# Optimization experiments

Hardware: AMD Instinct MI355X
Metric: run time of the kernel (lower is better)

The kernel has to match this reference:

```python
import jax, jax.numpy as jnp
import numpy as np
import math

NUM_CONVS = 4
GN_GROUPS = 32
GN_EPS = 1e-5
FPN_STRIDES = (8, 16, 32, 64, 128)
PRIOR_PROB = 0.01


def conv3x3(x, w, b):
    # x: [N,C,H,W], w: [O,I,3,3]
    y = jax.lax.conv_general_dilated(
        x, w, window_strides=(1, 1), padding='SAME',
        dimension_numbers=('NCHW', 'OIHW', 'NCHW'))
    return y + b[None, :, None, None]


def group_norm(x, gamma, beta):
    n, c, h, w = x.shape
    xg = x.reshape(n, GN_GROUPS, c // GN_GROUPS, h, w)
    mean = xg.mean(axis=(2, 3, 4), keepdims=True)
    var = xg.var(axis=(2, 3, 4), keepdims=True)
    xn = ((xg - mean) * jax.lax.rsqrt(var + GN_EPS)).reshape(n, c, h, w)
    return xn * gamma[None, :, None, None] + beta[None, :, None, None]


def subnet(x, ws, bs, gws, gbs):
    # NUM_CONVS x (conv3x3 -> GN -> ReLU)
    for i in range(NUM_CONVS):
        x = jax.nn.relu(group_norm(conv3x3(x, ws[i], bs[i]), gws[i], gbs[i]))
    return x


def permute_to_N_HWA_K(x, k):
    n = x.shape[0]
    return x.transpose(0, 2, 3, 1).reshape(n, -1, k)


def setup_inputs() -> dict:
    key = jax.random.key(0)
    ks = jax.random.split(key, 16)
    C, K = 256, 80
    feats = {
        'p3': jax.random.normal(ks[0], (1, C, 80, 80), jnp.float32),
        'p4': jax.random.normal(ks[1], (1, C, 40, 40), jnp.float32),
        'p5': jax.random.normal(ks[2], (1, C, 20, 20), jnp.float32),
        'p6': jax.random.normal(ks[3], (1, C, 10, 10), jnp.float32),
        'p7': jax.random.normal(ks[4], (1, C, 5, 5), jnp.float32),
    }
    std = 0.01
    bias_value = -math.log((1 - PRIOR_PROB) / PRIOR_PROB)
    params = {
        'cls_w': std * jax.random.normal(ks[5], (NUM_CONVS, C, C, 3, 3), jnp.float32),
        'cls_b': jnp.zeros((NUM_CONVS, C), jnp.float32),
        'cls_gn_w': jnp.ones((NUM_CONVS, C), jnp.float32),
        'cls_gn_b': jnp.zeros((NUM_CONVS, C), jnp.float32),
        'box_w': std * jax.random.normal(ks[6], (NUM_CONVS, C, C, 3, 3), jnp.float32),
        'box_b': jnp.zeros((NUM_CONVS, C), jnp.float32),
        'box_gn_w': jnp.ones((NUM_CONVS, C), jnp.float32),
        'box_gn_b': jnp.zeros((NUM_CONVS, C), jnp.float32),
        'score_w': std * jax.random.normal(ks[7], (K, C, 3, 3), jnp.float32),
        'score_b': jnp.full((K,), bias_value, jnp.float32),
        'pred_w': std * jax.random.normal(ks[8], (4, C, 3, 3), jnp.float32),
        'pred_b': jnp.zeros((4,), jnp.float32),
        'iou_w': std * jax.random.normal(ks[9], (1, C, 3, 3), jnp.float32),
        'iou_b': jnp.zeros((1,), jnp.float32),
        'scales': jnp.ones((5,), jnp.float32),
    }
    return {**feats, **params}


def reference(p3, p4, p5, p6, p7,
              cls_w, cls_b, cls_gn_w, cls_gn_b,
              box_w, box_b, box_gn_w, box_gn_b,
              score_w, score_b, pred_w, pred_b, iou_w, iou_b, scales):
    features = [p3, p4, p5, p6, p7]
    logits, bbox_reg, ious = [], [], []
    for l, feat in enumerate(features):
        c = subnet(feat, cls_w, cls_b, cls_gn_w, cls_gn_b)
        b = subnet(feat, box_w, box_b, box_gn_w, box_gn_b)
        logit = conv3x3(c, score_w, score_b)          # [N,80,H,W]
        iou = conv3x3(b, iou_w, iou_b)                # [N,1,H,W]
        bp = conv3x3(b, pred_w, pred_b) * scales[l]   # Scale module
        # norm_reg_targets=True branch
        reg = jax.nn.relu(bp) * FPN_STRIDES[l]        # [N,4,H,W]
        logits.append(permute_to_N_HWA_K(logit, 80))
        bbox_reg.append(permute_to_N_HWA_K(reg, 4))
        ious.append(permute_to_N_HWA_K(iou, 1))
    box_cls = jnp.concatenate(logits, axis=1)    # [N, sumHW, 80]
    box_delta = jnp.concatenate(bbox_reg, axis=1)  # [N, sumHW, 4]
    box_iou = jnp.concatenate(ious, axis=1)      # [N, sumHW, 1]
    # pack into one array for a single output: [N, sumHW, 85]
    return jnp.concatenate([box_cls, box_delta, box_iou], axis=-1)
```

## Files before the change

### kernel.cpp

```cpp
#include <hip/hip_runtime.h>

typedef unsigned short u16;
typedef __attribute__((ext_vector_type(8))) short bf16x8;
typedef __attribute__((ext_vector_type(4))) float f32x4;

#define NLEV 5
#define CCH 256
#define KTOT 2304
#define P_TOT 8525
#define PP_TOT 9165

__constant__ int   c_HW[NLEV]     = {6400, 1600, 400, 100, 25};
__constant__ int   c_W[NLEV]      = {80, 40, 20, 10, 5};
__constant__ int   c_off[NLEV]    = {0, 6400, 8000, 8400, 8500};
__constant__ int   c_poff[NLEV]   = {0, 6724, 8488, 8972, 9116};
__constant__ int   c_pts[NLEV+1]  = {0, 100, 125, 132, 134, 135};
__constant__ float c_stridef[NLEV]= {8.f, 16.f, 32.f, 64.f, 128.f};

__device__ __forceinline__ u16 f2bf(float f){
  union { float f; unsigned u; } v; v.f = f;
  unsigned r = v.u + 0x7fffu + ((v.u >> 16) & 1u);
  return (u16)(r >> 16);
}

__device__ __forceinline__ void g2l16(const u16* g, u16* l, int lane){
#if defined(__has_builtin)
#if __has_builtin(__builtin_amdgcn_global_load_lds)
  __builtin_amdgcn_global_load_lds(
      (const __attribute__((address_space(1))) unsigned int*)g,
      (__attribute__((address_space(3))) unsigned int*)l, 16, 0, 0);
  return;
#endif
#endif
  *(uint4*)(l + lane*8) = *(const uint4*)g;
}

#define WAIT_VM0   0x0F70
#define WAIT_LGKM0 0xC07F

template<int MODE>
__global__ __launch_bounds__(256, 2) void gemm_conv(
    const u16* __restrict__ Xc, const u16* __restrict__ Xb,
    const u16* __restrict__ Wc, const u16* __restrict__ Wb,
    const float* __restrict__ bc, const float* __restrict__ bb,
    float* __restrict__ Yc, float* __restrict__ Yb,
    float* __restrict__ stats,
    const float* __restrict__ predb, const float* __restrict__ ioub,
    const float* __restrict__ scales, float* __restrict__ out)
{
  __shared__ u16 sbuf[4*8192];
  __shared__ float sstat[32][2];

  const int ptile = blockIdx.x, br = blockIdx.z;
  const int tid = threadIdx.x, wv = tid >> 6, ln = tid & 63;

  if (MODE == 1) {
    if (br == 0 ? (wv >= 2) : (wv >= 1)) return;
  }

  int lv = 0;
  #pragma unroll
  for (int i = 1; i < NLEV; i++) if (ptile >= c_pts[i]) lv = i;
  const int ptl = ptile - c_pts[lv];
  const int HW = c_HW[lv], Wl = c_W[lv], wrow = Wl + 2;
  const int quad = ln >> 4, l15 = ln & 15;
  const int lr = ln >> 3;
  const int gsw = (ln & 7) ^ lr;

  const u16* __restrict__ X  = br ? Xb : Xc;
  const u16* __restrict__ WA = br ? Wb : Wc;

  u16* myA = &sbuf[wv * 8192];
  u16* myB = myA + 4096;

  const u16* aptr[8]; const u16* bptr[8];
  #pragma unroll
  for (int j = 0; j < 8; j++)
    aptr[j] = WA + (size_t)(wv*64 + j*8 + lr) * KTOT + gsw*8;
  #pragma unroll
  for (int j = 0; j < 8; j++) {
    const int p = ptl*64 + j*8 + lr;
    int pb = 0;
    if (p < HW) { const int h = p / Wl, wi = p - h*Wl; pb = h*wrow + wi; }
    bptr[j] = X + (size_t)(c_poff[lv] + pb) * CCH + gsw*8;
  }

  auto stage = [&](int s) {
    const int tap = s >> 2;
    const int dh = tap / 3, dw = tap - dh*3;
    const int aof = s * 64;
    const int bof = (dh*wrow + dw)*CCH + ((s & 3) << 6);
    #pragma unroll
    for (int j = 0; j < 8; j++) g2l16(aptr[j] + aof, myA + j*512, ln);
    #pragma unroll
    for (int j = 0; j < 8; j++) g2l16(bptr[j] + bof, myB + j*512, ln);
  };

  f32x4 acc[4][4];
  #pragma unroll
  for (int i = 0; i < 4; i++)
    #pragma unroll
    for (int j = 0; j < 4; j++) acc[i][j] = (f32x4){0.f, 0.f, 0.f, 0.f};

  stage(0);
  #pragma unroll 1
  for (int s = 0; s < 36; s++) {
    __builtin_amdgcn_s_waitcnt(WAIT_VM0);
    bf16x8 af[2][4], bf[2][4];
    #pragma unroll
    for (int sub = 0; sub < 2; sub++) {
      const int ga = ((sub*4 + quad) ^ (l15 & 7)) * 8;
      #pragma unroll
      for (int t = 0; t < 4; t++) {
        af[sub][t] = *(const bf16x8*)&myA[(t*16 + l15)*64 + ga];
        bf[sub][t] = *(const bf16x8*)&myB[(t*16 + l15)*64 + ga];
      }
    }
    __builtin_amdgcn_s_waitcnt(WAIT_LGKM0);
    if (s < 35) stage(s + 1);
    #pragma unroll
    for (int sub = 0; sub < 2; sub++)
      #pragma unroll
      for (int mt = 0; mt < 4; mt++)
        #pragma unroll
        for (int nt = 0; nt < 4; nt++)
          acc[mt][nt] = __builtin_amdgcn_mfma_f32_16x16x32_bf16(
              af[sub][mt], bf[sub][nt], acc[mt][nt], 0, 0, 0);
  }

  const int nrem = HW - ptl*64;
  if (MODE == 0) {
    if (tid < 64) sstat[tid >> 1][tid & 1] = 0.f;
    __syncthreads();
    const float* __restrict__ bias = br ? bb : bc;
    float* __restrict__ Y = br ? Yb : Yc;
    #pragma unroll
    for (int mt = 0; mt < 4; mt++) {
      const int mrow = wv*64 + mt*16 + quad*4;
      const f32x4 bv = *(const f32x4*)&bias[mrow];
      float s = 0.f, sq = 0.f;
      #pragma unroll
      for (int nt = 0; nt < 4; nt++) {
        const int nl = nt*16 + l15;
        f32x4 v = acc[mt][nt] + bv;
        if (nl < nrem) {
          const size_t n = (size_t)(c_off[lv] + ptl*64 + nl);
          *(f32x4*)&Y[n*CCH + mrow] = v;
          #pragma unroll
          for (int r = 0; r < 4; r++) { s += v[r]; sq += v[r]*v[r]; }
        }
      }
      #pragma unroll
      for (int o = 1; o < 16; o <<= 1) { s += __shfl_xor(s, o); sq += __shfl_xor(sq, o); }
      if (l15 == 0) {
        const int g = mrow >> 3;
        atomicAdd(&sstat[g][0], s);
        atomicAdd(&sstat[g][1], sq);
      }
    }
    __syncthreads();
    if (tid < 64) {
      const int g = tid >> 1, c = tid & 1;
      atomicAdd(&stats[((br*NLEV + lv)*32 + g)*2 + c], sstat[g][c]);
    }
  } else {
    const float scl = scales[lv];
    const float stf = c_stridef[lv];
    #pragma unroll
    for (int mt = 0; mt < 4; mt++) {
      const int mr0 = wv*64 + mt*16 + quad*4;
      if (mr0 >= 85) continue;
      #pragma unroll
      for (int nt = 0; nt < 4; nt++) {
        const int nl = nt*16 + l15;
        if (nl >= nrem) continue;
        const size_t n = (size_t)(c_off[lv] + ptl*64 + nl);
        const f32x4 v = acc[mt][nt];
        #pragma unroll
        for (int r = 0; r < 4; r++) {
          const int m = mr0 + r;
          if (br == 0) {
            if (m < 80) out[n*85 + m] = v[r] + bc[m];
          } else {
            if (m < 4) {
              const float t = (v[r] + predb[m]) * scl;
              out[n*85 + 80 + m] = fmaxf(t, 0.f) * stf;
            } else if (m == 4) {
              out[n*85 + 84] = v[r] + ioub[0];
            }
          }
        }
      }
    }
  }
}

__global__ __launch_bounds__(256) void gn_relu(
    const float* __restrict__ Yc, const float* __restrict__ Yb,
    const float* __restrict__ stats,
    const float* __restrict__ gwc, const float* __restrict__ gbc,
    const float* __restrict__ gwb, const float* __restrict__ gbb,
    u16* __restrict__ Xc, u16* __restrict__ Xb)
{
  const int t = blockIdx.x * 256 + threadIdx.x;
  if (t >= 2 * P_TOT * 32) return;
  const int br = t / (P_TOT * 32);
  const int r  = t - br * (P_TOT * 32);
  const int pg = r >> 5;
  const int c0 = (r & 31) << 3;
  int lv = 0;
  #pragma unroll
  for (int i = 1; i < NLEV; i++) if (pg >= c_off[i]) lv = i;
  const int pl = pg - c_off[lv];
  const int Wl = c_W[lv];
  const int g = c0 >> 3;
  const float* st = &stats[(((size_t)br*NLEV + lv)*32 + g)*2];
  const float cnt = 8.f * (float)c_HW[lv];
  const float mean = st[0] / cnt;
  const float var  = st[1] / cnt - mean*mean;
  const float rstd = rsqrtf(var + 1e-5f);
  const float* Y  = br ? Yb : Yc;
  const float* gw = br ? gwb : gwc;
  const float* gb = br ? gbb : gbc;
  u16* X = br ? Xb : Xc;
  const float* y = &Y[(size_t)pg*CCH + c0];
  const int h = pl / Wl, wi = pl - h*Wl;
  const size_t pidx = (size_t)(c_poff[lv] + (h+1)*(Wl+2) + (wi+1));
  union { u16 u[8]; uint4 v; } pk;
  #pragma unroll
  for (int i = 0; i < 8; i++) {
    const float v = (y[i] - mean)*rstd*gw[c0+i] + gb[c0+i];
    pk.u[i] = f2bf(fmaxf(v, 0.f));
  }
  *(uint4*)&X[pidx*CCH + c0] = pk.v;
}

__global__ __launch_bounds__(256) void feat2bf(
    const float* __restrict__ p3, const float* __restrict__ p4,
    const float* __restrict__ p5, const float* __restrict__ p6,
    const float* __restrict__ p7, u16* __restrict__ X)
{
  const int t = blockIdx.x * 256 + threadIdx.x;
  if (t >= P_TOT * 32) return;
  const int pg = t >> 5, c0 = (t & 31) << 3;
  int lv = 0;
  #pragma unroll
  for (int i = 1; i < NLEV; i++) if (pg >= c_off[i]) lv = i;
  const int pl = pg - c_off[lv];
  const float* src = lv==0 ? p3 : lv==1 ? p4 : lv==2 ? p5 : lv==3 ? p6 : p7;
  const int HW = c_HW[lv], Wl = c_W[lv];
  const int h = pl / Wl, wi = pl - h*Wl;
  const size_t pidx = (size_t)(c_poff[lv] + (h+1)*(Wl+2) + (wi+1));
  union { u16 u[8]; uint4 v; } pk;
  #pragma unroll
  for (int i = 0; i < 8; i++)
    pk.u[i] = f2bf(src[(size_t)(c0+i)*HW + pl]);
  *(uint4*)&X[pidx*CCH + c0] = pk.v;
}

__global__ __launch_bounds__(256) void wconv(
    const float* __restrict__ cw, const float* __restrict__ bw,
    u16* __restrict__ Wc, u16* __restrict__ Wb)
{
  const size_t N = (size_t)4*256*KTOT;
  const size_t t = (size_t)blockIdx.x * 256 + threadIdx.x;
  if (t >= 2*N) return;
  const float* src = (t < N) ? cw : bw;
  u16* dst = (t < N) ? Wc : Wb;
  const size_t i = (t < N) ? t : t - N;
  const size_t lc = i / KTOT;
  const int kk = (int)(i - lc*KTOT);
  const int tap = kk >> 8, ci = kk & 255;
  dst[i] = f2bf(src[(lc*256 + ci)*9 + tap]);
}

__global__ __launch_bounds__(256) void hconv(
    const float* __restrict__ sw, const float* __restrict__ pw,
    const float* __restrict__ iw, u16* __restrict__ Whc, u16* __restrict__ Whb)
{
  const int N = 128 * KTOT;
  const int t = blockIdx.x * 256 + threadIdx.x;
  if (t >= 2*N) return;
  const int i = (t < N) ? t : t - N;
  const int co = i / KTOT, kk = i - co*KTOT;
  const int tap = kk >> 8, ci = kk & 255;
  float v = 0.f;
  if (t < N) {
    if (co < 80) v = sw[(co*256 + ci)*9 + tap];
    Whc[i] = f2bf(v);
  } else {
    if (co < 4)       v = pw[(co*256 + ci)*9 + tap];
    else if (co == 4) v = iw[ci*9 + tap];
    Whb[i] = f2bf(v);
  }
}

extern "C" void kernel_launch(void* const* d_in, const int* in_sizes, int n_in,
                              void* d_out, int out_size, void* d_ws, size_t ws_size,
                              hipStream_t stream)
{
  const float* p3      = (const float*)d_in[0];
  const float* p4      = (const float*)d_in[1];
  const float* p5      = (const float*)d_in[2];
  const float* p6      = (const float*)d_in[3];
  const float* p7      = (const float*)d_in[4];
  const float* cls_w   = (const float*)d_in[5];
  const float* cls_b   = (const float*)d_in[6];
  const float* cls_gw  = (const float*)d_in[7];
  const float* cls_gb  = (const float*)d_in[8];
  const float* box_w   = (const float*)d_in[9];
  const float* box_b   = (const float*)d_in[10];
  const float* box_gw  = (const float*)d_in[11];
  const float* box_gb  = (const float*)d_in[12];
  const float* score_w = (const float*)d_in[13];
  const float* score_b = (const float*)d_in[14];
  const float* pred_w  = (const float*)d_in[15];
  const float* pred_b  = (const float*)d_in[16];
  const float* iou_w   = (const float*)d_in[17];
  const float* iou_b   = (const float*)d_in[18];
  const float* scales  = (const float*)d_in[19];
  float* out = (float*)d_out;

  char* w = (char*)d_ws;
  size_t o = 0;
  auto alloc = [&](size_t b) { void* p = w + o; o += (b + 255) & ~(size_t)255; return p; };
  u16*   XF = (u16*)alloc((size_t)PP_TOT*CCH*2);
  u16*   XC = (u16*)alloc((size_t)PP_TOT*CCH*2);
  u16*   XB = (u16*)alloc((size_t)PP_TOT*CCH*2);
  float* ST = (float*)alloc((size_t)4*2*NLEV*32*2*4);
  u16*  WRC = (u16*)alloc((size_t)4*256*KTOT*2);
  u16*  WRB = (u16*)alloc((size_t)4*256*KTOT*2);
  u16*  WHC = (u16*)alloc((size_t)128*KTOT*2);
  u16*  WHB = (u16*)alloc((size_t)128*KTOT*2);
  float* YC = (float*)alloc((size_t)P_TOT*CCH*4);
  float* YB = (float*)alloc((size_t)P_TOT*CCH*4);

  hipMemsetAsync(XF, 0, (size_t)3*PP_TOT*CCH*2 + (size_t)4*2*NLEV*32*2*4, stream);

  wconv<<<dim3((unsigned)(((size_t)2*4*256*KTOT + 255)/256)), 256, 0, stream>>>(cls_w, box_w, WRC, WRB);
  hconv<<<dim3((2*128*KTOT + 255)/256), 256, 0, stream>>>(score_w, pred_w, iou_w, WHC, WHB);
  feat2bf<<<dim3((P_TOT*32 + 255)/256), 256, 0, stream>>>(p3, p4, p5, p6, p7, XF);

  const u16* xci = XF; const u16* xbi = XF;
  for (int l = 0; l < 4; l++) {
    float* STl = ST + (size_t)l*2*NLEV*32*2;
    gemm_conv<0><<<dim3(135, 1, 2), 256, 0, stream>>>(
        xci, xbi, WRC + (size_t)l*256*KTOT, WRB + (size_t)l*256*KTOT,
        cls_b + l*256, box_b + l*256, YC, YB, STl,
        nullptr, nullptr, nullptr, nullptr);
    gn_relu<<<dim3((2*P_TOT*32 + 255)/256), 256, 0, stream>>>(
        YC, YB, STl, cls_gw + l*256, cls_gb + l*256, box_gw + l*256, box_gb + l*256,
        XC, XB);
    xci = XC; xbi = XB;
  }
  gemm_conv<1><<<dim3(135, 1, 2), 256, 0, stream>>>(
      xci, xbi, WHC, WHB, score_b, nullptr, nullptr, nullptr, nullptr,
      pred_b, iou_b, scales, out);
}
```

Measured before the change: 396.6 us.

## Share 128x128 LDS tiles across waves with double buffering and blocked layouts

The conv GEMM moves from per-wave private 64x64 tiles to a block-shared 128(M)x128(N) tile. All four waves cooperatively load A and B into double-buffered LDS and synchronise with a barrier each stage, so each loaded tile is reused across waves. Weights are pre-swizzled into a stage-blocked layout, and activations are stored channel-blocked in groups of 64, so each stage's loads are contiguous. This cuts redundant global and LDS traffic per output, but adds a per-stage barrier and reduces the block count (69x2x2 for the body convs, 69x1x2 for the heads), which may hurt occupancy on the small levels.

```diff
diff --git a/kernel.cpp b/kernel.cpp
--- a/kernel.cpp
+++ b/kernel.cpp
@@ -9,12 +9,13 @@
 #define KTOT 2304
 #define P_TOT 8525
 #define PP_TOT 9165
+#define PLS (PP_TOT*64)
 
 __constant__ int   c_HW[NLEV]     = {6400, 1600, 400, 100, 25};
 __constant__ int   c_W[NLEV]      = {80, 40, 20, 10, 5};
 __constant__ int   c_off[NLEV]    = {0, 6400, 8000, 8400, 8500};
 __constant__ int   c_poff[NLEV]   = {0, 6724, 8488, 8972, 9116};
-__constant__ int   c_pts[NLEV+1]  = {0, 100, 125, 132, 134, 135};
+__constant__ int   c_pts[NLEV+1]  = {0, 50, 63, 67, 68, 69};
 __constant__ float c_stridef[NLEV]= {8.f, 16.f, 32.f, 64.f, 128.f};
 
 __device__ __forceinline__ u16 f2bf(float f){
@@ -35,8 +36,7 @@
   *(uint4*)(l + lane*8) = *(const uint4*)g;
 }
 
-#define WAIT_VM0   0x0F70
-#define WAIT_LGKM0 0xC07F
+#define WAIT_VM0_LGKM0 0x0070
 
 template<int MODE>
 __global__ __launch_bounds__(256, 2) void gemm_conv(
@@ -48,52 +48,46 @@
     const float* __restrict__ predb, const float* __restrict__ ioub,
     const float* __restrict__ scales, float* __restrict__ out)
 {
-  __shared__ u16 sbuf[4*8192];
-  __shared__ float sstat[32][2];
-
-  const int ptile = blockIdx.x, br = blockIdx.z;
-  const int tid = threadIdx.x, wv = tid >> 6, ln = tid & 63;
-
-  if (MODE == 1) {
-    if (br == 0 ? (wv >= 2) : (wv >= 1)) return;
-  }
-
+  __shared__ u16 sA0[8192], sB0[8192], sA1[8192], sB1[8192];
+  __shared__ float sstat[16][2];
+
+  const int ptile = blockIdx.x, mtile = blockIdx.y, br = blockIdx.z;
   int lv = 0;
   #pragma unroll
   for (int i = 1; i < NLEV; i++) if (ptile >= c_pts[i]) lv = i;
   const int ptl = ptile - c_pts[lv];
   const int HW = c_HW[lv], Wl = c_W[lv], wrow = Wl + 2;
+  const int tid = threadIdx.x, wv = tid >> 6, ln = tid & 63;
   const int quad = ln >> 4, l15 = ln & 15;
-  const int lr = ln >> 3;
-  const int gsw = (ln & 7) ^ lr;
+  const int m0w = (wv & 1) * 64, n0w = (wv >> 1) * 64;
 
   const u16* __restrict__ X  = br ? Xb : Xc;
   const u16* __restrict__ WA = br ? Wb : Wc;
 
-  u16* myA = &sbuf[wv * 8192];
-  u16* myB = myA + 4096;
-
-  const u16* aptr[8]; const u16* bptr[8];
-  #pragma unroll
-  for (int j = 0; j < 8; j++)
-    aptr[j] = WA + (size_t)(wv*64 + j*8 + lr) * KTOT + gsw*8;
-  #pragma unroll
-  for (int j = 0; j < 8; j++) {
-    const int p = ptl*64 + j*8 + lr;
+  const int ASTRIDE = (MODE == 0) ? 16384 : 8192;
+  const u16* abase = WA + (size_t)(((MODE == 0) ? mtile*16 : 0) + wv*4)*512 + ln*8;
+
+  const int bsw = ((ln & 7) ^ ((ln >> 3) & 7)) * 8;
+  const u16* bsrc[4];
+  #pragma unroll
+  for (int i = 0; i < 4; i++) {
+    const int p = ptl*128 + wv*32 + i*8 + (ln >> 3);
     int pb = 0;
     if (p < HW) { const int h = p / Wl, wi = p - h*Wl; pb = h*wrow + wi; }
-    bptr[j] = X + (size_t)(c_poff[lv] + pb) * CCH + gsw*8;
-  }
-
-  auto stage = [&](int s) {
-    const int tap = s >> 2;
+    bsrc[i] = X + (size_t)(c_poff[lv] + pb) * 64 + bsw;
+  }
+
+  auto stage = [&](int s, u16* dA, u16* dB) {
+    const int tap = s >> 2, cc = s & 3;
     const int dh = tap / 3, dw = tap - dh*3;
-    const int aof = s * 64;
-    const int bof = (dh*wrow + dw)*CCH + ((s & 3) << 6);
-    #pragma unroll
-    for (int j = 0; j < 8; j++) g2l16(aptr[j] + aof, myA + j*512, ln);
-    #pragma unroll
-    for (int j = 0; j < 8; j++) g2l16(bptr[j] + bof, myB + j*512, ln);
+    const u16* as = abase + (size_t)s * ASTRIDE;
+    const int bsh = cc * PLS + (dh*wrow + dw) * 64;
+    u16* da = dA + (wv*4)*512;
+    u16* db = dB + (wv*4)*512;
+    #pragma unroll
+    for (int i = 0; i < 4; i++) g2l16(as + i*512, da + i*512, ln);
+    #pragma unroll
+    for (int i = 0; i < 4; i++) g2l16(bsrc[i] + bsh, db + i*512, ln);
   };
 
   f32x4 acc[4][4];
@@ -102,22 +96,24 @@
     #pragma unroll
     for (int j = 0; j < 4; j++) acc[i][j] = (f32x4){0.f, 0.f, 0.f, 0.f};
 
-  stage(0);
-  #pragma unroll 1
-  for (int s = 0; s < 36; s++) {
-    __builtin_amdgcn_s_waitcnt(WAIT_VM0);
+  if (MODE == 0 && tid < 32) sstat[tid >> 1][tid & 1] = 0.f;
+
+  auto kbody = [&](int s, const u16* rA, const u16* rB, u16* wA2, u16* wB2) {
+    __builtin_amdgcn_s_waitcnt(WAIT_VM0_LGKM0);
+    __builtin_amdgcn_sched_barrier(0);
+    __builtin_amdgcn_s_barrier();
+    __builtin_amdgcn_sched_barrier(0);
+    if (s < 35) stage(s + 1, wA2, wB2);
     bf16x8 af[2][4], bf[2][4];
     #pragma unroll
     for (int sub = 0; sub < 2; sub++) {
-      const int ga = ((sub*4 + quad) ^ (l15 & 7)) * 8;
       #pragma unroll
       for (int t = 0; t < 4; t++) {
-        af[sub][t] = *(const bf16x8*)&myA[(t*16 + l15)*64 + ga];
-        bf[sub][t] = *(const bf16x8*)&myB[(t*16 + l15)*64 + ga];
+        const int swz = ((sub*4 + quad) ^ (l15 & 7)) * 8;
+        af[sub][t] = *(const bf16x8*)&rA[(m0w + t*16 + l15)*64 + swz];
+        bf[sub][t] = *(const bf16x8*)&rB[(n0w + t*16 + l15)*64 + swz];
       }
     }
-    __builtin_amdgcn_s_waitcnt(WAIT_LGKM0);
-    if (s < 35) stage(s + 1);
     #pragma unroll
     for (int sub = 0; sub < 2; sub++)
       #pragma unroll
@@ -126,25 +122,31 @@
         for (int nt = 0; nt < 4; nt++)
           acc[mt][nt] = __builtin_amdgcn_mfma_f32_16x16x32_bf16(
               af[sub][mt], bf[sub][nt], acc[mt][nt], 0, 0, 0);
-  }
-
-  const int nrem = HW - ptl*64;
+  };
+
+  stage(0, sA0, sB0);
+  #pragma unroll 1
+  for (int s = 0; s < 36; s += 2) {
+    kbody(s,     sA0, sB0, sA1, sB1);
+    kbody(s + 1, sA1, sB1, sA0, sB0);
+  }
+
+  const int nrem = HW - ptl*128;
   if (MODE == 0) {
-    if (tid < 64) sstat[tid >> 1][tid & 1] = 0.f;
-    __syncthreads();
     const float* __restrict__ bias = br ? bb : bc;
     float* __restrict__ Y = br ? Yb : Yc;
     #pragma unroll
     for (int mt = 0; mt < 4; mt++) {
-      const int mrow = wv*64 + mt*16 + quad*4;
+      const int mloc = m0w + mt*16 + quad*4;
+      const int mrow = mtile*128 + mloc;
       const f32x4 bv = *(const f32x4*)&bias[mrow];
       float s = 0.f, sq = 0.f;
       #pragma unroll
       for (int nt = 0; nt < 4; nt++) {
-        const int nl = nt*16 + l15;
+        const int nl = n0w + nt*16 + l15;
         f32x4 v = acc[mt][nt] + bv;
         if (nl < nrem) {
-          const size_t n = (size_t)(c_off[lv] + ptl*64 + nl);
+          const size_t n = (size_t)(c_off[lv] + ptl*128 + nl);
           *(f32x4*)&Y[n*CCH + mrow] = v;
           #pragma unroll
           for (int r = 0; r < 4; r++) { s += v[r]; sq += v[r]*v[r]; }
@@ -153,28 +155,28 @@
       #pragma unroll
       for (int o = 1; o < 16; o <<= 1) { s += __shfl_xor(s, o); sq += __shfl_xor(sq, o); }
       if (l15 == 0) {
-        const int g = mrow >> 3;
+        const int g = mloc >> 3;
         atomicAdd(&sstat[g][0], s);
         atomicAdd(&sstat[g][1], sq);
       }
     }
     __syncthreads();
-    if (tid < 64) {
+    if (tid < 32) {
       const int g = tid >> 1, c = tid & 1;
-      atomicAdd(&stats[((br*NLEV + lv)*32 + g)*2 + c], sstat[g][c]);
+      atomicAdd(&stats[((br*NLEV + lv)*32 + mtile*16 + g)*2 + c], sstat[g][c]);
     }
   } else {
     const float scl = scales[lv];
     const float stf = c_stridef[lv];
     #pragma unroll
     for (int mt = 0; mt < 4; mt++) {
-      const int mr0 = wv*64 + mt*16 + quad*4;
+      const int mr0 = m0w + mt*16 + quad*4;
       if (mr0 >= 85) continue;
       #pragma unroll
       for (int nt = 0; nt < 4; nt++) {
-        const int nl = nt*16 + l15;
+        const int nl = n0w + nt*16 + l15;
         if (nl >= nrem) continue;
-        const size_t n = (size_t)(c_off[lv] + ptl*64 + nl);
+        const size_t n = (size_t)(c_off[lv] + ptl*128 + nl);
         const f32x4 v = acc[mt][nt];
         #pragma unroll
         for (int r = 0; r < 4; r++) {
@@ -232,7 +234,7 @@
     const float v = (y[i] - mean)*rstd*gw[c0+i] + gb[c0+i];
     pk.u[i] = f2bf(fmaxf(v, 0.f));
   }
-  *(uint4*)&X[pidx*CCH + c0] = pk.v;
+  *(uint4*)&X[(size_t)(c0 >> 6)*PLS + pidx*64 + (c0 & 63)] = pk.v;
 }
 
 __global__ __launch_bounds__(256) void feat2bf(
@@ -255,7 +257,7 @@
   #pragma unroll
   for (int i = 0; i < 8; i++)
     pk.u[i] = f2bf(src[(size_t)(c0+i)*HW + pl]);
-  *(uint4*)&X[pidx*CCH + c0] = pk.v;
+  *(uint4*)&X[(size_t)(c0 >> 6)*PLS + pidx*64 + (c0 & 63)] = pk.v;
 }
 
 __global__ __launch_bounds__(256) void wconv(
@@ -270,8 +272,13 @@
   const size_t i = (t < N) ? t : t - N;
   const size_t lc = i / KTOT;
   const int kk = (int)(i - lc*KTOT);
+  const int l = (int)(lc >> 8), co = (int)(lc & 255);
   const int tap = kk >> 8, ci = kk & 255;
-  dst[i] = f2bf(src[(lc*256 + ci)*9 + tap]);
+  const int s = kk >> 6, kl = kk & 63;
+  const int r = co & 7, p = (kl >> 3) ^ r;
+  const size_t d = (size_t)l*589824 +
+      ((size_t)((s*32 + (co >> 3))*64 + r*8 + p))*8 + (kl & 7);
+  dst[d] = f2bf(src[(lc*256 + ci)*9 + tap]);
 }
 
 __global__ __launch_bounds__(256) void hconv(
@@ -284,14 +291,17 @@
   const int i = (t < N) ? t : t - N;
   const int co = i / KTOT, kk = i - co*KTOT;
   const int tap = kk >> 8, ci = kk & 255;
+  const int s = kk >> 6, kl = kk & 63;
+  const int r = co & 7, p = (kl >> 3) ^ r;
+  const size_t d = ((size_t)((s*16 + (co >> 3))*64 + r*8 + p))*8 + (kl & 7);
   float v = 0.f;
   if (t < N) {
     if (co < 80) v = sw[(co*256 + ci)*9 + tap];
-    Whc[i] = f2bf(v);
+    Whc[d] = f2bf(v);
   } else {
     if (co < 4)       v = pw[(co*256 + ci)*9 + tap];
     else if (co == 4) v = iw[ci*9 + tap];
-    Whb[i] = f2bf(v);
+    Whb[d] = f2bf(v);
   }
 }
 
@@ -344,8 +354,8 @@
   const u16* xci = XF; const u16* xbi = XF;
   for (int l = 0; l < 4; l++) {
     float* STl = ST + (size_t)l*2*NLEV*32*2;
-    gemm_conv<0><<<dim3(135, 1, 2), 256, 0, stream>>>(
-        xci, xbi, WRC + (size_t)l*256*KTOT, WRB + (size_t)l*256*KTOT,
+    gemm_conv<0><<<dim3(69, 2, 2), 256, 0, stream>>>(
+        xci, xbi, WRC + (size_t)l*589824, WRB + (size_t)l*589824,
         cls_b + l*256, box_b + l*256, YC, YB, STl,
         nullptr, nullptr, nullptr, nullptr);
     gn_relu<<<dim3((2*P_TOT*32 + 255)/256), 256, 0, stream>>>(
@@ -353,7 +363,7 @@
         XC, XB);
     xci = XC; xbi = XB;
   }
-  gemm_conv<1><<<dim3(135, 1, 2), 256, 0, stream>>>(
+  gemm_conv<1><<<dim3(69, 1, 2), 256, 0, stream>>>(
       xci, xbi, WHC, WHB, score_b, nullptr, nullptr, nullptr, nullptr,
       pred_b, iou_b, scales, out);
 }
```

Measured after the change: 367.6 us. -7.3%, faster.
